# Kernel tuning notes

Hardware: AMD Instinct MI355X
Metric: run time of the kernel (lower is better)

Reference implementation:

```python
import jax, jax.numpy as jnp
import numpy as np

B, H, L, D = 16, 8, 128, 64
SCALE = jnp.float32(np.sqrt(D))
NEG = jnp.float32(-1e9)


def setup_inputs() -> dict:
    key = jax.random.key(0)
    kq, kk, kv, km = jax.random.split(key, 4)
    Q = jax.random.normal(kq, (B, H, L, D), dtype=jnp.float32)
    K = jax.random.normal(kk, (H, B, L, D), dtype=jnp.float32)
    V = jax.random.normal(kv, (H, B, L, D), dtype=jnp.float32)
    mask = jax.random.randint(km, (B, 1, 1, L, L), 0, 2, dtype=jnp.int32)
    return {"Q": Q, "K": K, "V": V, "mask": mask}


def reference(Q, K, V, mask):
    # Cross-sample (intersample) attention:
    # scores[b,h,c,i,j] = <Q[b,h,i,:], K[h,c,j,:]> / sqrt(D)  -> (B,H,B,L,L)
    scores = jnp.einsum('bhid,hcjd->bhcij', Q, K) / SCALE
    scores = jnp.where(mask == 0, NEG, scores)
    attn_weights = jax.nn.softmax(scores, axis=-1)  # (B,H,B,L,L)
    # output[b,h,c,i,:] = sum_j w[b,h,c,i,j] * V[h,c,j,:]  -> (B,H,B,L,D)
    output = jnp.einsum('bhcij,hcjd->bhcid', attn_weights, V)
    return (output, attn_weights)
```

## Files before the change

### kernel.cpp

```cpp
#include <hip/hip_runtime.h>
#include <hip/hip_bf16.h>

typedef float  f32x4  __attribute__((ext_vector_type(4)));
typedef __bf16 bf16x8 __attribute__((ext_vector_type(8)));

#define MFMA16(A,B,C) __builtin_amdgcn_mfma_f32_16x16x32_bf16((A),(B),(C),0,0,0)

constexpr int BN = 16, HN = 8, LN = 128, DN = 64;
constexpr size_t OUT0 = (size_t)BN * HN * BN * LN * DN;

constexpr int KTS = 72;
constexpr int VTS = 136;
constexpr int PS  = 36;

__device__ __forceinline__ void load8_split(const float* __restrict__ p, float scale,
                                            bf16x8& hi, bf16x8& lo) {
  float f[8];
  *(float4*)&f[0] = *(const float4*)(p);
  *(float4*)&f[4] = *(const float4*)(p + 4);
#pragma unroll
  for (int i = 0; i < 8; ++i) {
    float x = f[i] * scale;
    __bf16 h = (__bf16)x;
    hi[i] = h;
    lo[i] = (__bf16)(x - (float)h);
  }
}

__device__ __forceinline__ void lds8_split(const float* p, bf16x8& hi, bf16x8& lo) {
  float f[8];
  *(float4*)&f[0] = *(const float4*)(p);
  *(float4*)&f[4] = *(const float4*)(p + 4);
#pragma unroll
  for (int i = 0; i < 8; ++i) {
    __bf16 h = (__bf16)f[i];
    hi[i] = h;
    lo[i] = (__bf16)(f[i] - (float)h);
  }
}

__global__ __launch_bounds__(256, 3) void isa_attn_kernel(
    const float* __restrict__ Q, const float* __restrict__ K,
    const float* __restrict__ V, const int* __restrict__ M,
    float* __restrict__ out)
{
  __shared__ __bf16 KT[LN * KTS];
  __shared__ __bf16 VT[DN * VTS];
  __shared__ float  P [LN * PS];

  const int bid = blockIdx.x;
  const int w = (bid & 7) * 256 + (bid >> 3);
  const int h = w >> 8;
  const int c = (w >> 4) & 15;
  const int b = w & 15;

  const float* Qp = Q + (size_t)(b * HN + h) * (LN * DN);
  const float* Kp = K + (size_t)(h * BN + c) * (LN * DN);
  const float* Vp = V + (size_t)(h * BN + c) * (LN * DN);
  const int*   Mp = M + (size_t)b * (LN * LN);
  float* Op = out + (size_t)((b * HN + h) * BN + c) * (LN * DN);
  float* Wp = out + OUT0 + (size_t)((b * HN + h) * BN + c) * (LN * LN);

  const int t    = threadIdx.x;
  const int lane = t & 63;
  const int wid  = t >> 6;
  const int quad = lane >> 4;
  const int l16  = lane & 15;
  const int row0 = wid * 32;

#pragma unroll
  for (int it = 0; it < 4; ++it) {
    int idx = t + it * 256;
    int n  = idx >> 3;
    int k0 = (idx & 7) * 8;
    float4 a0 = *(const float4*)(Kp + n * DN + k0);
    float4 a1 = *(const float4*)(Kp + n * DN + k0 + 4);
    bf16x8 kk;
    kk[0] = (__bf16)a0.x; kk[1] = (__bf16)a0.y; kk[2] = (__bf16)a0.z; kk[3] = (__bf16)a0.w;
    kk[4] = (__bf16)a1.x; kk[5] = (__bf16)a1.y; kk[6] = (__bf16)a1.z; kk[7] = (__bf16)a1.w;
    *(bf16x8*)&KT[n * KTS + k0] = kk;
  }

  {
    int j8 = t >> 4;
    int d0 = (t & 15) * 4;
    float4 vv[8];
#pragma unroll
    for (int r = 0; r < 8; ++r)
      vv[r] = *(const float4*)(Vp + (j8 * 8 + r) * DN + d0);
#pragma unroll
    for (int dw = 0; dw < 4; ++dw) {
      bf16x8 col;
#pragma unroll
      for (int r = 0; r < 8; ++r)
        col[r] = (__bf16)(((const float*)&vv[r])[dw]);
      *(bf16x8*)&VT[(d0 + dw) * VTS + j8 * 8] = col;
    }
  }

  bf16x8 qhi[2][2], qlo[2][2];
#pragma unroll
  for (int rt = 0; rt < 2; ++rt)
#pragma unroll
    for (int kt = 0; kt < 2; ++kt)
      load8_split(Qp + (row0 + rt * 16 + l16) * DN + kt * 32 + quad * 8, 0.125f,
                  qhi[rt][kt], qlo[rt][kt]);

  __syncthreads();

  f32x4 acc[2][8];
#pragma unroll
  for (int rt = 0; rt < 2; ++rt)
#pragma unroll
    for (int ct = 0; ct < 8; ++ct)
      acc[rt][ct] = (f32x4){0.f, 0.f, 0.f, 0.f};

#pragma unroll
  for (int ct = 0; ct < 8; ++ct) {
#pragma unroll
    for (int kt = 0; kt < 2; ++kt) {
      bf16x8 kh = *(const bf16x8*)&KT[(ct * 16 + l16) * KTS + kt * 32 + quad * 8];
#pragma unroll
      for (int rt = 0; rt < 2; ++rt) {
        acc[rt][ct] = MFMA16(qhi[rt][kt], kh, acc[rt][ct]);
        acc[rt][ct] = MFMA16(qlo[rt][kt], kh, acc[rt][ct]);
      }
    }
  }

#pragma unroll
  for (int rt = 0; rt < 2; ++rt) {
#pragma unroll
    for (int r = 0; r < 4; ++r) {
      int row = row0 + rt * 16 + quad * 4 + r;
      const int* mrow = Mp + (size_t)row * LN + l16;
      float mf[8];
#pragma unroll
      for (int ct = 0; ct < 8; ++ct) mf[ct] = (float)mrow[ct * 16];
      float mx = -3.0e38f;
#pragma unroll
      for (int ct = 0; ct < 8; ++ct) mx = fmaxf(mx, acc[rt][ct][r]);
      mx = fmaxf(mx, __shfl_xor(mx, 1));
      mx = fmaxf(mx, __shfl_xor(mx, 2));
      mx = fmaxf(mx, __shfl_xor(mx, 4));
      mx = fmaxf(mx, __shfl_xor(mx, 8));
      float s[8];
      float sum = 0.f;
#pragma unroll
      for (int ct = 0; ct < 8; ++ct) {
        s[ct] = __expf(acc[rt][ct][r] - mx) * mf[ct];
        sum += s[ct];
      }
      sum += __shfl_xor(sum, 1);
      sum += __shfl_xor(sum, 2);
      sum += __shfl_xor(sum, 4);
      sum += __shfl_xor(sum, 8);
      float inv = __builtin_amdgcn_rcpf(sum);
      inv = inv * (2.0f - sum * inv);
#pragma unroll
      for (int ct = 0; ct < 8; ++ct) acc[rt][ct][r] = s[ct] * inv;
    }
  }

  f32x4 oacc[2][4];
#pragma unroll
  for (int rt = 0; rt < 2; ++rt)
#pragma unroll
    for (int nt = 0; nt < 4; ++nt)
      oacc[rt][nt] = (f32x4){0.f, 0.f, 0.f, 0.f};

#pragma unroll
  for (int qu = 0; qu < 4; ++qu) {
#pragma unroll
    for (int rt = 0; rt < 2; ++rt)
#pragma unroll
      for (int cc = 0; cc < 2; ++cc)
#pragma unroll
        for (int r = 0; r < 4; ++r)
          P[(row0 + rt * 16 + quad * 4 + r) * PS + cc * 16 + l16] =
              acc[rt][qu * 2 + cc][r];

#pragma unroll
    for (int e = 0; e < 4; ++e) {
      int idx = e * 64 + lane;
      int rl  = idx >> 3;
      int c4  = idx & 7;
      float4 v = *(const float4*)&P[(row0 + rl) * PS + c4 * 4];
      *(float4*)&Wp[(size_t)(row0 + rl) * LN + qu * 32 + c4 * 4] = v;
    }

    bf16x8 phi[2], plo[2];
#pragma unroll
    for (int rt = 0; rt < 2; ++rt)
      lds8_split(&P[(row0 + rt * 16 + l16) * PS + quad * 8], phi[rt], plo[rt]);
#pragma unroll
    for (int nt = 0; nt < 4; ++nt) {
      bf16x8 vh = *(const bf16x8*)&VT[(nt * 16 + l16) * VTS + qu * 32 + quad * 8];
#pragma unroll
      for (int rt = 0; rt < 2; ++rt) {
        oacc[rt][nt] = MFMA16(phi[rt], vh, oacc[rt][nt]);
        oacc[rt][nt] = MFMA16(plo[rt], vh, oacc[rt][nt]);
      }
    }
  }

#pragma unroll
  for (int hf = 0; hf < 2; ++hf) {
#pragma unroll
    for (int rt = 0; rt < 2; ++rt)
#pragma unroll
      for (int nn = 0; nn < 2; ++nn)
#pragma unroll
        for (int r = 0; r < 4; ++r)
          P[(row0 + rt * 16 + quad * 4 + r) * PS + nn * 16 + l16] =
              oacc[rt][hf * 2 + nn][r];
#pragma unroll
    for (int e = 0; e < 4; ++e) {
      int idx = e * 64 + lane;
      int rl  = idx >> 3;
      int c4  = idx & 7;
      float4 v = *(const float4*)&P[(row0 + rl) * PS + c4 * 4];
      *(float4*)&Op[(size_t)(row0 + rl) * DN + hf * 32 + c4 * 4] = v;
    }
  }
}

extern "C" void kernel_launch(void* const* d_in, const int* in_sizes, int n_in,
                              void* d_out, int out_size, void* d_ws, size_t ws_size,
                              hipStream_t stream) {
  const float* Q = (const float*)d_in[0];
  const float* K = (const float*)d_in[1];
  const float* V = (const float*)d_in[2];
  const int*   M = (const int*)d_in[3];
  isa_attn_kernel<<<dim3(BN * HN * BN), dim3(256), 0, stream>>>(Q, K, V, M, (float*)d_out);
}
```

Measured before the change: 239.7 us.

## Precompute bf16 Q/K/V in workspace and stream into swizzled LDS

Adds a pre-pass kernel that converts Q into scaled bf16 hi/lo halves, K into bf16 with an XOR swizzle, and V into transposed, swizzled bf16, all stored in workspace. The attention kernel then copies K/V tiles straight into LDS with global_load_lds and reads Q directly as bf16. This removes the conversions that every block used to repeat and halves K/V read bytes. It costs an extra kernel launch and a workspace round trip, and it falls back to the old kernel if the workspace is too small.

```diff
diff --git a/kernel.cpp b/kernel.cpp
--- a/kernel.cpp
+++ b/kernel.cpp
@@ -9,9 +9,13 @@
 constexpr int BN = 16, HN = 8, LN = 128, DN = 64;
 constexpr size_t OUT0 = (size_t)BN * HN * BN * LN * DN;
 
+constexpr int QE = BN * HN * LN * DN;
+constexpr size_t WS_BYTES = (size_t)4 * QE * sizeof(__bf16);
+
+constexpr int PS  = 36;
 constexpr int KTS = 72;
 constexpr int VTS = 136;
-constexpr int PS  = 36;
+
 
 __device__ __forceinline__ void load8_split(const float* __restrict__ p, float scale,
                                             bf16x8& hi, bf16x8& lo) {
@@ -36,6 +40,243 @@
     __bf16 h = (__bf16)f[i];
     hi[i] = h;
     lo[i] = (__bf16)(f[i] - (float)h);
+  }
+}
+
+__device__ __forceinline__ void gload_lds16(const void* g, void* l) {
+  __builtin_amdgcn_global_load_lds(
+      (const __attribute__((address_space(1))) unsigned int*)g,
+      (__attribute__((address_space(3))) unsigned int*)l, 16, 0, 0);
+}
+
+__global__ __launch_bounds__(256) void pre_kernel(
+    const float* __restrict__ Q, const float* __restrict__ K,
+    const float* __restrict__ V, __bf16* __restrict__ ws)
+{
+  const int t   = threadIdx.x;
+  const int blk = blockIdx.x;
+
+  if (blk < 512) {
+    int base = blk * 2048 + t * 8;
+    float f[8];
+    *(float4*)&f[0] = *(const float4*)(Q + base);
+    *(float4*)&f[4] = *(const float4*)(Q + base + 4);
+    bf16x8 hi, lo;
+#pragma unroll
+    for (int i = 0; i < 8; ++i) {
+      float x = f[i] * 0.125f;
+      __bf16 h = (__bf16)x;
+      hi[i] = h;
+      lo[i] = (__bf16)(x - (float)h);
+    }
+    *(bf16x8*)&ws[base]      = hi;
+    *(bf16x8*)&ws[QE + base] = lo;
+  } else if (blk < 1024) {
+    int g  = (blk - 512) * 256 + t;
+    int k0 = (g & 7) * 8;
+    int n  = (g >> 3) & 127;
+    int hc = g >> 10;
+    const float* src = K + ((size_t)hc * LN + n) * DN + k0;
+    float f[8];
+    *(float4*)&f[0] = *(const float4*)(src);
+    *(float4*)&f[4] = *(const float4*)(src + 4);
+    bf16x8 kk;
+#pragma unroll
+    for (int i = 0; i < 8; ++i) kk[i] = (__bf16)f[i];
+    int k0s = k0 ^ ((n & 7) << 3);
+    *(bf16x8*)&ws[2 * (size_t)QE + (size_t)hc * 8192 + n * 64 + k0s] = kk;
+  } else {
+    int hc = blk - 1024;
+    int j8 = t >> 4;
+    int d0 = (t & 15) * 4;
+    const float* Vp = V + (size_t)hc * (LN * DN);
+    float4 vv[8];
+#pragma unroll
+    for (int r = 0; r < 8; ++r)
+      vv[r] = *(const float4*)(Vp + (j8 * 8 + r) * DN + d0);
+#pragma unroll
+    for (int dw = 0; dw < 4; ++dw) {
+      int d = d0 + dw;
+      bf16x8 col;
+#pragma unroll
+      for (int r = 0; r < 8; ++r)
+        col[r] = (__bf16)(((const float*)&vv[r])[dw]);
+      int js = (j8 * 8) ^ ((d & 7) << 3);
+      *(bf16x8*)&ws[3 * (size_t)QE + (size_t)hc * 8192 + d * 128 + js] = col;
+    }
+  }
+}
+
+__global__ __launch_bounds__(256, 3) void isa_attn_fast(
+    const __bf16* __restrict__ ws, const int* __restrict__ M,
+    float* __restrict__ out)
+{
+  __shared__ __bf16 KT[LN * DN];
+  __shared__ __bf16 VT[DN * LN];
+  __shared__ float  P [LN * PS];
+
+  const int bid = blockIdx.x;
+  const int w = (bid & 7) * 256 + (bid >> 3);
+  const int h = w >> 8;
+  const int c = (w >> 4) & 15;
+  const int b = w & 15;
+  const int hc = h * BN + c;
+
+  const __bf16* Qh = ws + (size_t)(b * HN + h) * (LN * DN);
+  const __bf16* Ql = Qh + QE;
+  const __bf16* Ks = ws + 2 * (size_t)QE + (size_t)hc * 8192;
+  const __bf16* Vs = ws + 3 * (size_t)QE + (size_t)hc * 8192;
+  const int*   Mp = M + (size_t)b * (LN * LN);
+  float* Op = out + (size_t)((b * HN + h) * BN + c) * (LN * DN);
+  float* Wp = out + OUT0 + (size_t)((b * HN + h) * BN + c) * (LN * LN);
+
+  const int t    = threadIdx.x;
+  const int lane = t & 63;
+  const int wid  = t >> 6;
+  const int quad = lane >> 4;
+  const int l16  = lane & 15;
+  const int row0 = wid * 32;
+  const int swz  = (l16 & 7) << 3;
+
+  {
+    const char* kg = (const char*)Ks;
+    const char* vg = (const char*)Vs;
+    char* kl = (char*)KT;
+    char* vl = (char*)VT;
+#pragma unroll
+    for (int i = 0; i < 4; ++i)
+      gload_lds16(kg + t * 16 + i * 4096, kl + t * 16 + i * 4096);
+#pragma unroll
+    for (int i = 0; i < 4; ++i)
+      gload_lds16(vg + t * 16 + i * 4096, vl + t * 16 + i * 4096);
+  }
+
+  bf16x8 qhi[2][2], qlo[2][2];
+#pragma unroll
+  for (int rt = 0; rt < 2; ++rt)
+#pragma unroll
+    for (int kt = 0; kt < 2; ++kt) {
+      const int off = (row0 + rt * 16 + l16) * DN + kt * 32 + quad * 8;
+      qhi[rt][kt] = *(const bf16x8*)(Qh + off);
+      qlo[rt][kt] = *(const bf16x8*)(Ql + off);
+    }
+
+  __syncthreads();
+
+  f32x4 acc[2][8];
+#pragma unroll
+  for (int rt = 0; rt < 2; ++rt)
+#pragma unroll
+    for (int ct = 0; ct < 8; ++ct)
+      acc[rt][ct] = (f32x4){0.f, 0.f, 0.f, 0.f};
+
+#pragma unroll
+  for (int ct = 0; ct < 8; ++ct) {
+#pragma unroll
+    for (int kt = 0; kt < 2; ++kt) {
+      bf16x8 kh = *(const bf16x8*)&KT[(ct * 16 + l16) * 64 + ((kt * 32 + quad * 8) ^ swz)];
+#pragma unroll
+      for (int rt = 0; rt < 2; ++rt) {
+        acc[rt][ct] = MFMA16(qhi[rt][kt], kh, acc[rt][ct]);
+        acc[rt][ct] = MFMA16(qlo[rt][kt], kh, acc[rt][ct]);
+      }
+    }
+  }
+
+#pragma unroll
+  for (int rt = 0; rt < 2; ++rt) {
+#pragma unroll
+    for (int r = 0; r < 4; ++r) {
+      int row = row0 + rt * 16 + quad * 4 + r;
+      const int* mrow = Mp + (size_t)row * LN + l16;
+      float mf[8];
+#pragma unroll
+      for (int ct = 0; ct < 8; ++ct) mf[ct] = (float)mrow[ct * 16];
+      float mx = -3.0e38f;
+#pragma unroll
+      for (int ct = 0; ct < 8; ++ct) mx = fmaxf(mx, acc[rt][ct][r]);
+      mx = fmaxf(mx, __shfl_xor(mx, 1));
+      mx = fmaxf(mx, __shfl_xor(mx, 2));
+      mx = fmaxf(mx, __shfl_xor(mx, 4));
+      mx = fmaxf(mx, __shfl_xor(mx, 8));
+      float s[8];
+      float sum = 0.f;
+#pragma unroll
+      for (int ct = 0; ct < 8; ++ct) {
+        s[ct] = __expf(acc[rt][ct][r] - mx) * mf[ct];
+        sum += s[ct];
+      }
+      sum += __shfl_xor(sum, 1);
+      sum += __shfl_xor(sum, 2);
+      sum += __shfl_xor(sum, 4);
+      sum += __shfl_xor(sum, 8);
+      float inv = __builtin_amdgcn_rcpf(sum);
+      inv = inv * (2.0f - sum * inv);
+#pragma unroll
+      for (int ct = 0; ct < 8; ++ct) acc[rt][ct][r] = s[ct] * inv;
+    }
+  }
+
+  f32x4 oacc[2][4];
+#pragma unroll
+  for (int rt = 0; rt < 2; ++rt)
+#pragma unroll
+    for (int nt = 0; nt < 4; ++nt)
+      oacc[rt][nt] = (f32x4){0.f, 0.f, 0.f, 0.f};
+
+#pragma unroll
+  for (int qu = 0; qu < 4; ++qu) {
+#pragma unroll
+    for (int rt = 0; rt < 2; ++rt)
+#pragma unroll
+      for (int cc = 0; cc < 2; ++cc)
+#pragma unroll
+        for (int r = 0; r < 4; ++r)
+          P[(row0 + rt * 16 + quad * 4 + r) * PS + cc * 16 + l16] =
+              acc[rt][qu * 2 + cc][r];
+
+#pragma unroll
+    for (int e = 0; e < 4; ++e) {
+      int idx = e * 64 + lane;
+      int rl  = idx >> 3;
+      int c4  = idx & 7;
+      float4 v = *(const float4*)&P[(row0 + rl) * PS + c4 * 4];
+      *(float4*)&Wp[(size_t)(row0 + rl) * LN + qu * 32 + c4 * 4] = v;
+    }
+
+    bf16x8 phi[2], plo[2];
+#pragma unroll
+    for (int rt = 0; rt < 2; ++rt)
+      lds8_split(&P[(row0 + rt * 16 + l16) * PS + quad * 8], phi[rt], plo[rt]);
+#pragma unroll
+    for (int nt = 0; nt < 4; ++nt) {
+      bf16x8 vh = *(const bf16x8*)&VT[(nt * 16 + l16) * 128 + ((qu * 32 + quad * 8) ^ swz)];
+#pragma unroll
+      for (int rt = 0; rt < 2; ++rt) {
+        oacc[rt][nt] = MFMA16(phi[rt], vh, oacc[rt][nt]);
+        oacc[rt][nt] = MFMA16(plo[rt], vh, oacc[rt][nt]);
+      }
+    }
+  }
+
+#pragma unroll
+  for (int hf = 0; hf < 2; ++hf) {
+#pragma unroll
+    for (int rt = 0; rt < 2; ++rt)
+#pragma unroll
+      for (int nn = 0; nn < 2; ++nn)
+#pragma unroll
+        for (int r = 0; r < 4; ++r)
+          P[(row0 + rt * 16 + quad * 4 + r) * PS + nn * 16 + l16] =
+              oacc[rt][hf * 2 + nn][r];
+#pragma unroll
+    for (int e = 0; e < 4; ++e) {
+      int idx = e * 64 + lane;
+      int rl  = idx >> 3;
+      int c4  = idx & 7;
+      float4 v = *(const float4*)&P[(row0 + rl) * PS + c4 * 4];
+      *(float4*)&Op[(size_t)(row0 + rl) * DN + hf * 32 + c4 * 4] = v;
+    }
   }
 }
 
@@ -232,5 +473,11 @@
   const float* K = (const float*)d_in[1];
   const float* V = (const float*)d_in[2];
   const int*   M = (const int*)d_in[3];
-  isa_attn_kernel<<<dim3(BN * HN * BN), dim3(256), 0, stream>>>(Q, K, V, M, (float*)d_out);
-}
+  if (d_ws != nullptr && ws_size >= WS_BYTES) {
+    __bf16* ws = (__bf16*)d_ws;
+    pre_kernel<<<dim3(1152), dim3(256), 0, stream>>>(Q, K, V, ws);
+    isa_attn_fast<<<dim3(BN * HN * BN), dim3(256), 0, stream>>>(ws, M, (float*)d_out);
+  } else {
+    isa_attn_kernel<<<dim3(BN * HN * BN), dim3(256), 0, stream>>>(Q, K, V, M, (float*)d_out);
+  }
+}
```

Result: faster. 222.5 us (-7.2%).
